# Optimization experiments

Measured on AMD Instinct MI355X. Metric: run time of the kernel, lower is better.

Reference implementation:

```python
import jax, jax.numpy as jnp
import numpy as np

N_HEADS = 8
EPS = 1e-6


def setup_inputs() -> dict:
    key = jax.random.key(0)
    ks = jax.random.split(key, 9)
    B, L, E = 4, 4096, 512
    s = 1.0 / np.sqrt(E)
    return {
        "x": jax.random.normal(ks[0], (B, L, E), jnp.float32),
        "Wq": jax.random.normal(ks[1], (E, E), jnp.float32) * s,
        "bq": jax.random.normal(ks[2], (E,), jnp.float32) * 0.01,
        "Wk": jax.random.normal(ks[3], (E, E), jnp.float32) * s,
        "bk": jax.random.normal(ks[4], (E,), jnp.float32) * 0.01,
        "Wv": jax.random.normal(ks[5], (E, E), jnp.float32) * s,
        "bv": jax.random.normal(ks[6], (E,), jnp.float32) * 0.01,
        "Wo": jax.random.normal(ks[7], (E, E), jnp.float32) * s,
        "bo": jax.random.normal(ks[8], (E,), jnp.float32) * 0.01,
    }


def reference(x, Wq, bq, Wk, bk, Wv, bv, Wo, bo):
    # x: (B, L, E); self-attention so query = key = value = x
    B, L, E = x.shape
    H = N_HEADS
    d = E // H
    m = jnp.float32(L)  # m = max(src_len, tgt_len)

    # projections (torch Linear: x @ W.T + b), then ReLU feature map
    q = jax.nn.relu(x @ Wq.T + bq).reshape(B, L, H, d)
    k = jax.nn.relu(x @ Wk.T + bk).reshape(B, L, H, d)
    v = (x @ Wv.T + bv).reshape(B, L, H, d)

    # cosFormer positional reweighting: (pi/2) * i / m for i = 1..L
    idx = (jnp.pi / 2.0) * jnp.arange(1, L + 1, dtype=jnp.float32) / m  # (L,)
    sin = jnp.sin(idx)[None, :, None, None]  # (1, L, 1, 1)
    cos = jnp.cos(idx)[None, :, None, None]

    q_sin, q_cos = q * sin, q * cos
    k_sin, k_cos = k * sin, k * cos

    # non-causal linear attention: per-head kv state, O(L * d^2)
    kv_cos = jnp.einsum("blhk,blhd->bhkd", k_cos, v)  # (B, H, d, d)
    kv_sin = jnp.einsum("blhk,blhd->bhkd", k_sin, v)

    k_cos_sum = k_cos.sum(axis=1)  # (B, H, d)
    k_sin_sum = k_sin.sum(axis=1)

    z = 1.0 / jnp.maximum(
        jnp.einsum("blhd,bhd->blh", q_cos, k_cos_sum)
        + jnp.einsum("blhd,bhd->blh", q_sin, k_sin_sum),
        EPS,
    )  # (B, L, H)

    attn = (
        jnp.einsum("blhk,bhkd->blhd", q_cos, kv_cos)
        + jnp.einsum("blhk,bhkd->blhd", q_sin, kv_sin)
    ) * z[..., None]

    out = attn.reshape(B, L, E) @ Wo.T + bo  # (B, L, E)
    return out
```

## Files before the change

### kernel.cpp

```cpp
#include <hip/hip_runtime.h>
#include <hip/hip_bf16.h>

#define L_SEQ 4096
#define E_DIM 512
#define NHEAD 8
#define DHEAD 64
#define NBATCH 4
#define NROWS (NBATCH * L_SEQ)

typedef short bf16x8 __attribute__((ext_vector_type(8)));
typedef float f32x4 __attribute__((ext_vector_type(4)));

__device__ __forceinline__ float bf2f(ushort u) {
    union { float f; unsigned int i; } x;
    x.i = ((unsigned int)u) << 16;
    return x.f;
}
__device__ __forceinline__ ushort f2bf(float f) {
    unsigned int u = __float_as_uint(f);
    unsigned int r = 0x7fffu + ((u >> 16) & 1u);
    u += r;
    return (ushort)(u >> 16);
}

#define GLD16(gptr, lptr) \
    __builtin_amdgcn_global_load_lds( \
        (const __attribute__((address_space(1))) void*)(gptr), \
        (__attribute__((address_space(3))) void*)(lptr), 16, 0, 0)

#define BAR_LGKM() do { \
    asm volatile("s_waitcnt lgkmcnt(0)" ::: "memory"); \
    __builtin_amdgcn_sched_barrier(0); \
    __builtin_amdgcn_s_barrier(); \
    __builtin_amdgcn_sched_barrier(0); } while (0)

__global__ void convert_kernel(const float* __restrict__ in, ushort* __restrict__ out, int n4) {
    int stride = gridDim.x * blockDim.x;
    for (int i = blockIdx.x * blockDim.x + threadIdx.x; i < n4; i += stride) {
        float4 f = reinterpret_cast<const float4*>(in)[i];
        ushort4 o;
        o.x = f2bf(f.x); o.y = f2bf(f.y); o.z = f2bf(f.z); o.w = f2bf(f.w);
        reinterpret_cast<ushort4*>(out)[i] = o;
    }
}

__global__ __launch_bounds__(256) void convert_w_kernel(
    const float* __restrict__ w0, const float* __restrict__ w1,
    const float* __restrict__ w2, const float* __restrict__ w3,
    ushort* __restrict__ o0, ushort* __restrict__ o1,
    ushort* __restrict__ o2, ushort* __restrict__ o3,
    float* __restrict__ sintab, float* __restrict__ costab)
{
    const int tid = threadIdx.x;
    const int y = blockIdx.y;
    if (y == 4) {
        const int l = blockIdx.x * 256 + tid;
        if (blockIdx.x < 16) {
            const float ang = (float)(l + 1) * (1.5707963267948966f / (float)L_SEQ);
            sintab[l] = sinf(ang);
            costab[l] = cosf(ang);
        }
        return;
    }
    const float* in = (y == 0) ? w0 : (y == 1) ? w1 : (y == 2) ? w2 : w3;
    ushort* out = (y == 0) ? o0 : (y == 1) ? o1 : (y == 2) ? o2 : o3;
    const int i = blockIdx.x * 256 + tid;
    float4 f = reinterpret_cast<const float4*>(in)[i];
    ushort4 o;
    o.x = f2bf(f.x); o.y = f2bf(f.y); o.z = f2bf(f.z); o.w = f2bf(f.w);
    reinterpret_cast<ushort4*>(out)[i] = o;
}

template<int MODE_BASE>
__global__ __launch_bounds__(512) void gemm5_kernel(
    const ushort* __restrict__ A,
    const ushort* __restrict__ wq, const ushort* __restrict__ wk,
    const ushort* __restrict__ wv, const ushort* __restrict__ wo,
    const float* __restrict__ bq, const float* __restrict__ bk,
    const float* __restrict__ bv, const float* __restrict__ bo,
    ushort* __restrict__ qb, ushort* __restrict__ kT, ushort* __restrict__ vT,
    float* __restrict__ outF)
{
    __shared__ ushort SH[66048];
    ushort* TS = SH + 49152;

    const int tid = threadIdx.x;
    const int lane = tid & 63;
    const int wid = tid >> 6;
    const int wm = wid >> 2;
    const int wn = wid & 3;
    const int p = blockIdx.x;

    int mode, rowBase, colBase;
    if (MODE_BASE == 3) {
        mode = 3;
        rowBase = (p >> 1) * 128;
        colBase = (p & 1) * 256;
    } else {
        const int panel = p / 6;
        const int job = p - panel * 6;
        mode = job >> 1;
        colBase = (job & 1) * 256;
        rowBase = panel * 128;
    }

    const ushort* __restrict__ W =
        (mode == 0) ? wq : (mode == 1) ? wk : (mode == 2) ? wv : wo;
    const float* __restrict__ bias =
        (mode == 0) ? bq : (mode == 1) ? bk : (mode == 2) ? bv : bo;

    const int fr = lane & 15;
    const int g = lane >> 4;
    const int fr7 = fr & 7;
    const int sc_row = tid >> 3;
    const int sc_ch  = tid & 7;

    f32x4 acc[4][4];
#pragma unroll
    for (int m = 0; m < 4; ++m)
#pragma unroll
        for (int n = 0; n < 4; ++n)
            acc[m][n] = (f32x4){0.f, 0.f, 0.f, 0.f};

    auto STAGE = [&](int kt) {
        const int k0 = kt * 64;
        const int bufb = (kt & 1) * 24576;
#pragma unroll
        for (int i = 0; i < 2; ++i) {
            const int row = i * 64 + sc_row;
            const int srcc = (sc_ch ^ (row & 7)) * 8;
            GLD16(&A[(size_t)(rowBase + row) * E_DIM + k0 + srcc],
                  &SH[bufb + (i * 512 + tid) * 8]);
        }
#pragma unroll
        for (int i = 0; i < 4; ++i) {
            const int row = i * 64 + sc_row;
            const int srcc = (sc_ch ^ (row & 7)) * 8;
            GLD16(&W[(size_t)(colBase + row) * E_DIM + k0 + srcc],
                  &SH[bufb + 8192 + (i * 512 + tid) * 8]);
        }
    };

    STAGE(0);
    STAGE(1);
    asm volatile("s_waitcnt vmcnt(6)" ::: "memory");
    __builtin_amdgcn_sched_barrier(0);
    __builtin_amdgcn_s_barrier();
    __builtin_amdgcn_sched_barrier(0);

    const int kch0 = (g ^ fr7) * 8;
    const int kch1 = ((4 + g) ^ fr7) * 8;
    const int aroff = (wm * 64 + fr) * 64;
    const int broff = 8192 + (wn * 64 + fr) * 64;
    const int b = rowBase >> 12;
    const int lloc = rowBase & (L_SEQ - 1);

    for (int gt = 0; gt < 8; ++gt) {
        const int base = (gt & 1) * 24576;
        bf16x8 af[2][4], bfv[2][4];
#pragma unroll
        for (int m = 0; m < 4; ++m) {
            af[0][m] = *reinterpret_cast<const bf16x8*>(&SH[base + aroff + m * 1024 + kch0]);
            af[1][m] = *reinterpret_cast<const bf16x8*>(&SH[base + aroff + m * 1024 + kch1]);
        }
#pragma unroll
        for (int n = 0; n < 4; ++n) {
            bfv[0][n] = *reinterpret_cast<const bf16x8*>(&SH[base + broff + n * 1024 + kch0]);
            bfv[1][n] = *reinterpret_cast<const bf16x8*>(&SH[base + broff + n * 1024 + kch1]);
        }
        BAR_LGKM();

        if (gt + 2 < 8) STAGE(gt + 2);

        __builtin_amdgcn_s_setprio(1);
#pragma unroll
        for (int kk = 0; kk < 2; ++kk)
#pragma unroll
            for (int m = 0; m < 4; ++m)
#pragma unroll
                for (int n = 0; n < 4; ++n)
                    acc[m][n] = __builtin_amdgcn_mfma_f32_16x16x32_bf16(
                        af[kk][m], bfv[kk][n], acc[m][n], 0, 0, 0);
        __builtin_amdgcn_s_setprio(0);
        __builtin_amdgcn_sched_barrier(0);

        if (gt < 7) {
            if (gt + 2 < 8) asm volatile("s_waitcnt vmcnt(6)" ::: "memory");
            else            asm volatile("s_waitcnt vmcnt(0)" ::: "memory");
            __builtin_amdgcn_sched_barrier(0);
            __builtin_amdgcn_s_barrier();
            __builtin_amdgcn_sched_barrier(0);
        }
    }

    if (mode == 0) {
        const float* __restrict__ bq_ = bias;
#pragma unroll
        for (int m = 0; m < 4; ++m)
#pragma unroll
            for (int j = 0; j < 4; ++j) {
                const int grow = rowBase + wm * 64 + m * 16 + g * 4 + j;
#pragma unroll
                for (int n = 0; n < 4; ++n) {
                    const int gcol = colBase + wn * 64 + n * 16 + fr;
                    const float val = fmaxf(acc[m][n][j] + bq_[gcol], 0.f);
                    qb[(size_t)grow * E_DIM + gcol] = f2bf(val);
                }
            }
    } else if (mode == 3) {
#pragma unroll
        for (int m = 0; m < 4; ++m)
#pragma unroll
            for (int j = 0; j < 4; ++j) {
                const int grow = rowBase + wm * 64 + m * 16 + g * 4 + j;
#pragma unroll
                for (int n = 0; n < 4; ++n) {
                    const int gcol = colBase + wn * 64 + n * 16 + fr;
                    outF[(size_t)grow * E_DIM + gcol] = acc[m][n][j] + bias[gcol];
                }
            }
    } else {
        ushort* __restrict__ dstbuf = (mode == 1) ? kT : vT;
#pragma unroll
        for (int ph = 0; ph < 2; ++ph) {
            BAR_LGKM();
            if ((wn >> 1) == ph) {
#pragma unroll
                for (int m = 0; m < 4; ++m)
#pragma unroll
                    for (int j = 0; j < 4; ++j) {
                        const int lr_ = wm * 64 + m * 16 + g * 4 + j;
#pragma unroll
                        for (int n = 0; n < 4; ++n) {
                            const int fcl = (wn & 1) * 64 + n * 16 + fr;
                            float val = acc[m][n][j] + bias[colBase + ph * 128 + fcl];
                            if (mode == 1) val = fmaxf(val, 0.f);
                            TS[fcl * 132 + lr_] = f2bf(val);
                        }
                    }
            }
            BAR_LGKM();
#pragma unroll
            for (int i = 0; i < 4; ++i) {
                const int c = i * 512 + tid;
                const int r = c >> 4;
                const int cc = c & 15;
                const int gfeat = colBase + ph * 128 + r;
                const size_t dst = ((size_t)(b * E_DIM + gfeat)) * L_SEQ + lloc + cc * 8;
                *reinterpret_cast<uint4*>(&dstbuf[dst]) =
                    *reinterpret_cast<const uint4*>(&TS[r * 132 + cc * 8]);
            }
        }
    }
}

__global__ __launch_bounds__(256) void kv_kernel(
    const ushort* __restrict__ kT, const ushort* __restrict__ vT,
    const float* __restrict__ sintab, const float* __restrict__ costab,
    float* __restrict__ kv_part, float* __restrict__ sum_part)
{
    const int chunk = blockIdx.x;
    const int bh = blockIdx.y;
    const int tid = threadIdx.x;
    const int lane = tid & 63;
    const int w = tid >> 6;
    const int fr = lane & 15;
    const int g = lane >> 4;

    const size_t tbase = (size_t)bh * 64 * L_SEQ;

    f32x4 acc[8], accS[8];
#pragma unroll
    for (int n = 0; n < 8; ++n) {
        acc[n] = (f32x4){0.f, 0.f, 0.f, 0.f};
        accS[n] = (f32x4){0.f, 0.f, 0.f, 0.f};
    }

    const int lchunk = chunk * (L_SEQ / 8);
    for (int l0 = lchunk; l0 < lchunk + (L_SEQ / 8); l0 += 32) {
        const int col = l0 + g * 8;
        bf16x8 vf = *reinterpret_cast<const bf16x8*>(&vT[tbase + (size_t)(w * 16 + fr) * L_SEQ + col]);
        bf16x8 kf[4];
#pragma unroll
        for (int n = 0; n < 4; ++n)
            kf[n] = *reinterpret_cast<const bf16x8*>(&kT[tbase + (size_t)(n * 16 + fr) * L_SEQ + col]);
        float4 c0 = *reinterpret_cast<const float4*>(&costab[col]);
        float4 c1 = *reinterpret_cast<const float4*>(&costab[col + 4]);
        float4 s0 = *reinterpret_cast<const float4*>(&sintab[col]);
        float4 s1 = *reinterpret_cast<const float4*>(&sintab[col + 4]);
        const float c8[8] = {c0.x, c0.y, c0.z, c0.w, c1.x, c1.y, c1.z, c1.w};
        const float s8[8] = {s0.x, s0.y, s0.z, s0.w, s1.x, s1.y, s1.z, s1.w};
        bf16x8 afc, afs, cw, sw;
#pragma unroll
        for (int e = 0; e < 8; ++e) {
            const float v = bf2f((ushort)vf[e]);
            afc[e] = (short)f2bf(v * c8[e]);
            afs[e] = (short)f2bf(v * s8[e]);
            cw[e]  = (short)f2bf(c8[e]);
            sw[e]  = (short)f2bf(s8[e]);
        }
#pragma unroll
        for (int n = 0; n < 4; ++n) {
            acc[n]      = __builtin_amdgcn_mfma_f32_16x16x32_bf16(afc, kf[n], acc[n], 0, 0, 0);
            acc[n + 4]  = __builtin_amdgcn_mfma_f32_16x16x32_bf16(afs, kf[n], acc[n + 4], 0, 0, 0);
            accS[n]     = __builtin_amdgcn_mfma_f32_16x16x32_bf16(cw,  kf[n], accS[n], 0, 0, 0);
            accS[n + 4] = __builtin_amdgcn_mfma_f32_16x16x32_bf16(sw,  kf[n], accS[n + 4], 0, 0, 0);
        }
    }

    const size_t pbase = ((size_t)(chunk * 32 + bh)) * 8192;
#pragma unroll
    for (int n = 0; n < 8; ++n)
#pragma unroll
        for (int j = 0; j < 4; ++j)
            kv_part[pbase + (size_t)(w * 16 + g * 4 + j) * 128 + n * 16 + fr] = acc[n][j];
    if (w == 0 && g == 0) {
        const size_t sbase = (size_t)(chunk * 32 + bh) * 128;
#pragma unroll
        for (int n = 0; n < 8; ++n)
            sum_part[sbase + n * 16 + fr] = accS[n][0];
    }
}

#define KVT_ROWS 80
#define KVT_STRIDE (KVT_ROWS * 128)
__global__ __launch_bounds__(256) void kv_reduce_kernel(
    const float* __restrict__ kv_part, const float* __restrict__ sum_part,
    ushort* __restrict__ kvT)
{
    const int bh = blockIdx.x;
    const int tid = threadIdx.x;
    ushort* kvb = kvT + (size_t)bh * KVT_STRIDE;
    for (int idx = tid; idx < 8192; idx += 256) {
        float s = 0.f;
#pragma unroll
        for (int c = 0; c < 8; ++c)
            s += kv_part[((size_t)(c * 32 + bh)) * 8192 + idx];
        kvb[idx] = f2bf(s);
    }
    if (tid < 128) {
        float s = 0.f;
#pragma unroll
        for (int c = 0; c < 8; ++c)
            s += sum_part[(size_t)(c * 32 + bh) * 128 + tid];
        const ushort hi = f2bf(s);
        const float lo = s - bf2f(hi);
        kvb[64 * 128 + tid] = hi;
        kvb[65 * 128 + tid] = f2bf(lo);
    }
    for (int idx = tid; idx < 14 * 128; idx += 256)
        kvb[66 * 128 + idx] = 0;
}

__global__ __launch_bounds__(256) void attn_kernel(
    const ushort* __restrict__ Qb, const ushort* __restrict__ kvT,
    const float* __restrict__ sintab, const float* __restrict__ costab,
    ushort* __restrict__ attn_out)
{
    const int bh = blockIdx.y;
    const int b = bh >> 3, h = bh & 7;
    const int tid = threadIdx.x;
    const int lane = tid & 63;
    const int w = tid >> 6;

    __shared__ ushort Bs[KVT_ROWS][136];

#pragma unroll
    for (int i = 0; i < 5; ++i) {
        const int c = i * 256 + tid;
        const int d = c >> 4, cc = c & 15;
        *reinterpret_cast<uint4*>(&Bs[d][cc * 8]) =
            *reinterpret_cast<const uint4*>(&kvT[(size_t)bh * KVT_STRIDE + (size_t)c * 8]);
    }
    __syncthreads();

    const int rowBase = blockIdx.x * 256 + w * 64;
    const int fr = lane & 15;
    const int g = lane >> 4;

    float cvm[4], svm[4];
#pragma unroll
    for (int m = 0; m < 4; ++m) {
        const int l = (rowBase + m * 16 + fr) & (L_SEQ - 1);
        cvm[m] = costab[l];
        svm[m] = sintab[l];
    }

    f32x4 acc[4][5];
#pragma unroll
    for (int m = 0; m < 4; ++m)
#pragma unroll
        for (int n = 0; n < 5; ++n)
            acc[m][n] = (f32x4){0.f, 0.f, 0.f, 0.f};

#pragma unroll
    for (int ks = 0; ks < 4; ++ks) {
        const int kk = (ks & 1) * 32 + g * 8;
        const int kcomb = ks * 32 + g * 8;

        bf16x8 af[4];
#pragma unroll
        for (int m = 0; m < 4; ++m) {
            const int r = rowBase + m * 16 + fr;
            bf16x8 qf = *reinterpret_cast<const bf16x8*>(
                &Qb[((size_t)(b * L_SEQ) + r) * E_DIM + h * DHEAD + kk]);
            const float sc = (ks < 2) ? cvm[m] : svm[m];
#pragma unroll
            for (int e = 0; e < 8; ++e)
                af[m][e] = (short)f2bf(bf2f((ushort)qf[e]) * sc);
        }

        bf16x8 bfr[5];
#pragma unroll
        for (int n = 0; n < 5; ++n)
            bfr[n] = *reinterpret_cast<const bf16x8*>(&Bs[n * 16 + fr][kcomb]);
#pragma unroll
        for (int m = 0; m < 4; ++m)
#pragma unroll
            for (int n = 0; n < 5; ++n)
                acc[m][n] = __builtin_amdgcn_mfma_f32_16x16x32_bf16(af[m], bfr[n], acc[m][n], 0, 0, 0);
    }

#pragma unroll
    for (int m = 0; m < 4; ++m) {
#pragma unroll
        for (int j = 0; j < 4; ++j) {
            const float den = __shfl(acc[m][4][j], g * 16 + 0) + __shfl(acc[m][4][j], g * 16 + 1);
            const float z = 1.f / fmaxf(den, 1e-6f);
            const int grow = rowBase + m * 16 + g * 4 + j;
            const size_t obase = ((size_t)(b * L_SEQ) + grow) * E_DIM + h * DHEAD;
#pragma unroll
            for (int n = 0; n < 4; ++n)
                attn_out[obase + n * 16 + fr] = f2bf(acc[m][n][j] * z);
        }
    }
}

extern "C" void kernel_launch(void* const* d_in, const int* in_sizes, int n_in,
                              void* d_out, int out_size, void* d_ws, size_t ws_size,
                              hipStream_t stream) {
    const float* x  = (const float*)d_in[0];
    const float* Wq = (const float*)d_in[1];
    const float* bq = (const float*)d_in[2];
    const float* Wk = (const float*)d_in[3];
    const float* bk = (const float*)d_in[4];
    const float* Wv = (const float*)d_in[5];
    const float* bv = (const float*)d_in[6];
    const float* Wo = (const float*)d_in[7];
    const float* bo = (const float*)d_in[8];
    float* out = (float*)d_out;

    char* ws = (char*)d_ws;
    size_t off = 0;
    auto alloc = [&](size_t bytes) -> char* {
        char* p = ws + off;
        off += (bytes + 255) & ~(size_t)255;
        return p;
    };

    const size_t big = (size_t)NROWS * E_DIM * sizeof(ushort);
    ushort* xb  = (ushort*)alloc(big);
    ushort* wqb = (ushort*)alloc(512 * 512 * sizeof(ushort));
    ushort* wkb = (ushort*)alloc(512 * 512 * sizeof(ushort));
    ushort* wvb = (ushort*)alloc(512 * 512 * sizeof(ushort));
    ushort* wob = (ushort*)alloc(512 * 512 * sizeof(ushort));
    ushort* qb  = (ushort*)alloc(big);
    ushort* kT  = (ushort*)alloc(big);
    ushort* vT  = (ushort*)alloc(big);
    float* kv_part  = (float*)alloc((size_t)8 * 32 * 8192 * sizeof(float));
    float* sum_part = (float*)alloc((size_t)8 * 32 * 128 * sizeof(float));
    ushort* kvT     = (ushort*)alloc((size_t)32 * KVT_STRIDE * sizeof(ushort));
    float* sintab   = (float*)alloc(L_SEQ * sizeof(float));
    float* costab   = (float*)alloc(L_SEQ * sizeof(float));
    ushort* attnb = kT;

    convert_kernel<<<2048, 256, 0, stream>>>(x, xb, NROWS * E_DIM / 4);
    convert_w_kernel<<<dim3(256, 5), 256, 0, stream>>>(
        Wq, Wk, Wv, Wo, wqb, wkb, wvb, wob, sintab, costab);

    gemm5_kernel<0><<<768, 512, 0, stream>>>(
        xb, wqb, wkb, wvb, wob, bq, bk, bv, bo, qb, kT, vT, nullptr);

    kv_kernel<<<dim3(8, 32), 256, 0, stream>>>(kT, vT, sintab, costab, kv_part, sum_part);
    kv_reduce_kernel<<<32, 256, 0, stream>>>(kv_part, sum_part, kvT);

    attn_kernel<<<dim3(16, 32), 256, 0, stream>>>(qb, kvT, sintab, costab, attnb);

    gemm5_kernel<3><<<256, 512, 0, stream>>>(
        attnb, wqb, wkb, wvb, wob, bq, bk, bv, bo, nullptr, nullptr, nullptr, out);
}
```

Before: 108.4 us.

## Shrink GEMM tiles to 128x128 with 256-thread blocks for higher occupancy

The projection and output GEMMs move from 128x256 tiles on 512-thread blocks to 128x128 tiles on 256-thread blocks with a 2D grid. Shared memory drops to 64KB and launch bounds request two blocks per CU, so more blocks can overlap their loads and epilogues. The K/V transpose epilogue becomes a single pass through a padded staging tile. The cost is that each block loads a larger A panel relative to its output, so the activation matrix is re-read more often across column tiles.

```diff
diff --git a/kernel.cpp b/kernel.cpp
--- a/kernel.cpp
+++ b/kernel.cpp
@@ -72,7 +72,7 @@
 }
 
 template<int MODE_BASE>
-__global__ __launch_bounds__(512) void gemm5_kernel(
+__global__ __launch_bounds__(256, 2) void gemm6_kernel(
     const ushort* __restrict__ A,
     const ushort* __restrict__ wq, const ushort* __restrict__ wk,
     const ushort* __restrict__ wv, const ushort* __restrict__ wo,
@@ -81,28 +81,19 @@
     ushort* __restrict__ qb, ushort* __restrict__ kT, ushort* __restrict__ vT,
     float* __restrict__ outF)
 {
-    __shared__ ushort SH[66048];
-    ushort* TS = SH + 49152;
+    __shared__ ushort SH[32768];
+    ushort* TS = SH;
 
     const int tid = threadIdx.x;
     const int lane = tid & 63;
     const int wid = tid >> 6;
-    const int wm = wid >> 2;
-    const int wn = wid & 3;
-    const int p = blockIdx.x;
-
-    int mode, rowBase, colBase;
-    if (MODE_BASE == 3) {
-        mode = 3;
-        rowBase = (p >> 1) * 128;
-        colBase = (p & 1) * 256;
-    } else {
-        const int panel = p / 6;
-        const int job = p - panel * 6;
-        mode = job >> 1;
-        colBase = (job & 1) * 256;
-        rowBase = panel * 128;
-    }
+    const int wm = wid >> 1;
+    const int wn = wid & 1;
+    const int rowBase = blockIdx.x * 128;
+
+    int mode, colBase;
+    if (MODE_BASE == 3) { mode = 3; colBase = blockIdx.y * 128; }
+    else { mode = blockIdx.y >> 2; colBase = (blockIdx.y & 3) * 128; }
 
     const ushort* __restrict__ W =
         (mode == 0) ? wq : (mode == 1) ? wk : (mode == 2) ? wv : wo;
@@ -113,7 +104,7 @@
     const int g = lane >> 4;
     const int fr7 = fr & 7;
     const int sc_row = tid >> 3;
-    const int sc_ch  = tid & 7;
+    const int sc_c16 = tid & 7;
 
     f32x4 acc[4][4];
 #pragma unroll
@@ -124,26 +115,26 @@
 
     auto STAGE = [&](int kt) {
         const int k0 = kt * 64;
-        const int bufb = (kt & 1) * 24576;
-#pragma unroll
-        for (int i = 0; i < 2; ++i) {
-            const int row = i * 64 + sc_row;
-            const int srcc = (sc_ch ^ (row & 7)) * 8;
+        const int bufb = (kt & 1) * 16384;
+#pragma unroll
+        for (int i = 0; i < 4; ++i) {
+            const int row = i * 32 + sc_row;
+            const int srcc = (sc_c16 ^ (row & 7)) * 8;
             GLD16(&A[(size_t)(rowBase + row) * E_DIM + k0 + srcc],
-                  &SH[bufb + (i * 512 + tid) * 8]);
+                  &SH[bufb + row * 64 + sc_c16 * 8]);
         }
 #pragma unroll
         for (int i = 0; i < 4; ++i) {
-            const int row = i * 64 + sc_row;
-            const int srcc = (sc_ch ^ (row & 7)) * 8;
+            const int row = i * 32 + sc_row;
+            const int srcc = (sc_c16 ^ (row & 7)) * 8;
             GLD16(&W[(size_t)(colBase + row) * E_DIM + k0 + srcc],
-                  &SH[bufb + 8192 + (i * 512 + tid) * 8]);
+                  &SH[bufb + 8192 + row * 64 + sc_c16 * 8]);
         }
     };
 
     STAGE(0);
     STAGE(1);
-    asm volatile("s_waitcnt vmcnt(6)" ::: "memory");
+    asm volatile("s_waitcnt vmcnt(8)" ::: "memory");
     __builtin_amdgcn_sched_barrier(0);
     __builtin_amdgcn_s_barrier();
     __builtin_amdgcn_sched_barrier(0);
@@ -156,7 +147,7 @@
     const int lloc = rowBase & (L_SEQ - 1);
 
     for (int gt = 0; gt < 8; ++gt) {
-        const int base = (gt & 1) * 24576;
+        const int base = (gt & 1) * 16384;
         bf16x8 af[2][4], bfv[2][4];
 #pragma unroll
         for (int m = 0; m < 4; ++m) {
@@ -185,7 +176,7 @@
         __builtin_amdgcn_sched_barrier(0);
 
         if (gt < 7) {
-            if (gt + 2 < 8) asm volatile("s_waitcnt vmcnt(6)" ::: "memory");
+            if (gt + 2 < 8) asm volatile("s_waitcnt vmcnt(8)" ::: "memory");
             else            asm volatile("s_waitcnt vmcnt(0)" ::: "memory");
             __builtin_amdgcn_sched_barrier(0);
             __builtin_amdgcn_s_barrier();
@@ -194,7 +185,6 @@
     }
 
     if (mode == 0) {
-        const float* __restrict__ bq_ = bias;
 #pragma unroll
         for (int m = 0; m < 4; ++m)
 #pragma unroll
@@ -203,7 +193,7 @@
 #pragma unroll
                 for (int n = 0; n < 4; ++n) {
                     const int gcol = colBase + wn * 64 + n * 16 + fr;
-                    const float val = fmaxf(acc[m][n][j] + bq_[gcol], 0.f);
+                    const float val = fmaxf(acc[m][n][j] + bias[gcol], 0.f);
                     qb[(size_t)grow * E_DIM + gcol] = f2bf(val);
                 }
             }
@@ -221,35 +211,29 @@
             }
     } else {
         ushort* __restrict__ dstbuf = (mode == 1) ? kT : vT;
-#pragma unroll
-        for (int ph = 0; ph < 2; ++ph) {
-            BAR_LGKM();
-            if ((wn >> 1) == ph) {
-#pragma unroll
-                for (int m = 0; m < 4; ++m)
-#pragma unroll
-                    for (int j = 0; j < 4; ++j) {
-                        const int lr_ = wm * 64 + m * 16 + g * 4 + j;
-#pragma unroll
-                        for (int n = 0; n < 4; ++n) {
-                            const int fcl = (wn & 1) * 64 + n * 16 + fr;
-                            float val = acc[m][n][j] + bias[colBase + ph * 128 + fcl];
-                            if (mode == 1) val = fmaxf(val, 0.f);
-                            TS[fcl * 132 + lr_] = f2bf(val);
-                        }
-                    }
+        __syncthreads();
+#pragma unroll
+        for (int m = 0; m < 4; ++m)
+#pragma unroll
+            for (int j = 0; j < 4; ++j) {
+                const int lr_ = wm * 64 + m * 16 + g * 4 + j;
+#pragma unroll
+                for (int n = 0; n < 4; ++n) {
+                    const int fcl = wn * 64 + n * 16 + fr;
+                    float val = acc[m][n][j] + bias[colBase + fcl];
+                    if (mode == 1) val = fmaxf(val, 0.f);
+                    TS[fcl * 136 + lr_] = f2bf(val);
+                }
             }
-            BAR_LGKM();
-#pragma unroll
-            for (int i = 0; i < 4; ++i) {
-                const int c = i * 512 + tid;
-                const int r = c >> 4;
-                const int cc = c & 15;
-                const int gfeat = colBase + ph * 128 + r;
-                const size_t dst = ((size_t)(b * E_DIM + gfeat)) * L_SEQ + lloc + cc * 8;
-                *reinterpret_cast<uint4*>(&dstbuf[dst]) =
-                    *reinterpret_cast<const uint4*>(&TS[r * 132 + cc * 8]);
-            }
+        __syncthreads();
+#pragma unroll
+        for (int i = 0; i < 8; ++i) {
+            const int c = i * 256 + tid;
+            const int r = c >> 4;
+            const int cc = c & 15;
+            const size_t dst = ((size_t)(b * E_DIM + colBase + r)) * L_SEQ + lloc + cc * 8;
+            *reinterpret_cast<uint4*>(&dstbuf[dst]) =
+                *reinterpret_cast<const uint4*>(&TS[r * 136 + cc * 8]);
         }
     }
 }
@@ -478,7 +462,7 @@
     convert_w_kernel<<<dim3(256, 5), 256, 0, stream>>>(
         Wq, Wk, Wv, Wo, wqb, wkb, wvb, wob, sintab, costab);
 
-    gemm5_kernel<0><<<768, 512, 0, stream>>>(
+    gemm6_kernel<0><<<dim3(128, 12), 256, 0, stream>>>(
         xb, wqb, wkb, wvb, wob, bq, bk, bv, bo, qb, kT, vT, nullptr);
 
     kv_kernel<<<dim3(8, 32), 256, 0, stream>>>(kT, vT, sintab, costab, kv_part, sum_part);
@@ -486,6 +470,6 @@
 
     attn_kernel<<<dim3(16, 32), 256, 0, stream>>>(qb, kvT, sintab, costab, attnb);
 
-    gemm5_kernel<3><<<256, 512, 0, stream>>>(
+    gemm6_kernel<3><<<dim3(128, 4), 256, 0, stream>>>(
         attnb, wqb, wkb, wvb, wob, bq, bk, bv, bo, nullptr, nullptr, nullptr, out);
 }
```

After: 97.40 us. -10.1%, faster.
